# Kernel optimization log

Measured on AMD Instinct MI355X. Metric: run time of the kernel, lower is better.

## Reference

```python
import jax, jax.numpy as jnp
import numpy as np

N, E, G = 200000, 600000, 1024
NF_IN, EF_IN, H = 32, 16, 512
BN_EPS = 1e-5


def _bn(x, gamma, beta):
    # eval-mode BatchNorm1d with running_mean=0, running_var=1
    return x * (gamma / jnp.sqrt(1.0 + BN_EPS)) + beta


def setup_inputs() -> dict:
    key = jax.random.key(0)
    ks = jax.random.split(key, 32)
    s = 0.05
    inp = {
        'nf': jax.random.normal(ks[0], (N, NF_IN), jnp.float32),
        'ef': jax.random.normal(ks[1], (E, EF_IN), jnp.float32),
        'gf': jax.random.normal(ks[2], (G, H), jnp.float32),
        'device_params': jax.random.uniform(ks[3], (N,), jnp.float32),
        'node_y': jax.random.randint(ks[4], (N,), 0, 9),
        'batch_idx': jnp.sort(jax.random.randint(ks[5], (N,), 0, G)),
        'edge_index': jax.random.randint(ks[6], (2, E), 0, N),
        'nf_w1': jax.random.normal(ks[7], (NF_IN + 9, H), jnp.float32) * s,
        'nf_b1': jax.random.normal(ks[8], (H,), jnp.float32) * s,
        'nf_g1': jax.random.uniform(ks[9], (H,), jnp.float32, 0.5, 1.5),
        'nf_be1': jax.random.normal(ks[10], (H,), jnp.float32) * s,
        'nf_w2': jax.random.normal(ks[11], (H, H), jnp.float32) * s,
        'nf_b2': jax.random.normal(ks[12], (H,), jnp.float32) * s,
        'ef_w1': jax.random.normal(ks[13], (EF_IN, H), jnp.float32) * s,
        'ef_b1': jax.random.normal(ks[14], (H,), jnp.float32) * s,
        'ef_g1': jax.random.uniform(ks[15], (H,), jnp.float32, 0.5, 1.5),
        'ef_be1': jax.random.normal(ks[16], (H,), jnp.float32) * s,
        'ef_w2': jax.random.normal(ks[17], (H, H), jnp.float32) * s,
        'ef_b2': jax.random.normal(ks[18], (H,), jnp.float32) * s,
        'ow1': jax.random.normal(ks[19], (H, H), jnp.float32) * s,
        'ob1': jax.random.normal(ks[20], (H,), jnp.float32) * s,
        'og1': jax.random.uniform(ks[21], (H,), jnp.float32, 0.5, 1.5),
        'obe1': jax.random.normal(ks[22], (H,), jnp.float32) * s,
        'ow2': jax.random.normal(ks[23], (H, H), jnp.float32) * s,
        'ob2': jax.random.normal(ks[24], (H,), jnp.float32) * s,
        'og2': jax.random.uniform(ks[25], (H,), jnp.float32, 0.5, 1.5),
        'obe2': jax.random.normal(ks[26], (H,), jnp.float32) * s,
        'ow3': jax.random.normal(ks[27], (H, 2), jnp.float32) * s,
        'ob3': jax.random.normal(ks[28], (2,), jnp.float32) * s,
    }
    return inp


def reference(nf, ef, gf, device_params, node_y, batch_idx, edge_index,
              nf_w1, nf_b1, nf_g1, nf_be1, nf_w2, nf_b2,
              ef_w1, ef_b1, ef_g1, ef_be1, ef_w2, ef_b2,
              ow1, ob1, og1, obe1, ow2, ob2, og2, obe2, ow3, ob3):
    num_graphs = gf.shape[0]
    gelu = lambda x: jax.nn.gelu(x, approximate=False)  # torch nn.GELU default

    # DeviceParam_MLP: augment node features with scaled one-hot of node class
    nf_aug = jnp.concatenate(
        [nf, jax.nn.one_hot(node_y, 9, dtype=nf.dtype) * device_params[:, None]],
        axis=-1)  # [N, nf_in+9]
    h_n = gelu(_bn(nf_aug @ nf_w1 + nf_b1, nf_g1, nf_be1)) @ nf_w2 + nf_b2  # [N,H]
    h_e = gelu(_bn(ef @ ef_w1 + ef_b1, ef_g1, ef_be1)) @ ef_w2 + ef_b2      # [E,H]

    # two scatter_add pools into graph features
    gh = gf
    gh = gh + jax.ops.segment_sum(h_n, batch_idx, num_segments=num_graphs)
    edge_graph = batch_idx[edge_index[0]]  # graph id of each edge's source node
    gh = gh + jax.ops.segment_sum(h_e, edge_graph, num_segments=num_graphs)

    # output MLP (layer_num=3): two hidden blocks + final Linear -> 2
    x = gelu(_bn(gh @ ow1 + ob1, og1, obe1))
    x = gelu(_bn(x @ ow2 + ob2, og2, obe2))
    return x @ ow3 + ob3  # [G, 2]
```

## Files before the change

kernel.cpp:

```cpp
#include <hip/hip_runtime.h>
#include <hip/hip_bf16.h>

#define NN 200000
#define NE 600000
#define NG 1024
#define HH 512
#define ECAP 1024

typedef short short8 __attribute__((ext_vector_type(8)));
typedef float f32x4 __attribute__((ext_vector_type(4)));
typedef float f32x2 __attribute__((ext_vector_type(2)));
typedef float f32x16 __attribute__((ext_vector_type(16)));

__device__ __forceinline__ unsigned short f2bf(float f){
  unsigned u = __float_as_uint(f);
  u += 0x7fffu + ((u >> 16) & 1u);
  return (unsigned short)(u >> 16);
}
__device__ __forceinline__ float bf2f(unsigned short h){
  return __uint_as_float(((unsigned)h) << 16);
}

__device__ __forceinline__ short8 cvt8pk(float4 a, float4 b){
  union { short8 s; __hip_bfloat162 h[4]; } u;
  u.h[0] = __float22bfloat162_rn(make_float2(a.x, a.y));
  u.h[1] = __float22bfloat162_rn(make_float2(a.z, a.w));
  u.h[2] = __float22bfloat162_rn(make_float2(b.x, b.y));
  u.h[3] = __float22bfloat162_rn(make_float2(b.z, b.w));
  return u.s;
}

__device__ __forceinline__ void split8(const float* v, short8* hi, short8* lo){
  union { short8 s; __hip_bfloat162 h[4]; unsigned u[4]; } H, L;
#pragma unroll
  for (int p=0;p<4;++p){
    float a = v[2*p], b = v[2*p+1];
    H.h[p] = __float22bfloat162_rn(make_float2(a, b));
    unsigned hu = H.u[p];
    L.h[p] = __float22bfloat162_rn(make_float2(a - __uint_as_float(hu << 16),
                                               b - __uint_as_float(hu & 0xffff0000u)));
  }
  *hi = H.s; *lo = L.s;
}

__device__ __forceinline__ float gelu_f(float x){
  float p = __builtin_fmaf(x*x, -0.10294325f, -2.3022085f);
  float e = __builtin_amdgcn_exp2f(x * p);
  return x * __builtin_amdgcn_rcpf(1.0f + e);
}

__device__ __forceinline__ void g2(f32x2 xp, f32x2& aX, f32x2& aP,
    float C0, float C1, float C2, float C3, float C4, float C5, float C6, float C7){
  f32x2 s = __builtin_elementwise_fma(xp, xp, (f32x2)(-1.0f));
  f32x2 p = __builtin_elementwise_fma(s, (f32x2)C7, (f32x2)C6);
  p = __builtin_elementwise_fma(p, s, (f32x2)C5);
  p = __builtin_elementwise_fma(p, s, (f32x2)C4);
  p = __builtin_elementwise_fma(p, s, (f32x2)C3);
  p = __builtin_elementwise_fma(p, s, (f32x2)C2);
  p = __builtin_elementwise_fma(p, s, (f32x2)C1);
  p = __builtin_elementwise_fma(p, s, (f32x2)C0);
  aX += xp; aP += p;
}

#define ISQ 0.35355339059327376f
#define SQ2 1.41421356237309505f

__global__ __launch_bounds__(256) void kpre(
    const float* __restrict__ nfw1, const float* __restrict__ nfb1,
    const float* __restrict__ nfg1, const float* __restrict__ nfbe1,
    const float* __restrict__ efw1, const float* __restrict__ efb1,
    const float* __restrict__ efg1, const float* __restrict__ efbe1,
    unsigned short* __restrict__ w1n48T, unsigned short* __restrict__ w1eT16,
    float* __restrict__ b1n_s, float* __restrict__ b1e_s,
    const int* __restrict__ bidx, int* __restrict__ nstart,
    int* __restrict__ cnt, float* __restrict__ pcoef,
    const float* __restrict__ nf, const float* __restrict__ dp,
    const int* __restrict__ ny, const float* __restrict__ ef,
    unsigned short* __restrict__ nf48, unsigned short* __restrict__ efb){
  const float rs = 0.99999500003750f;
  int b = blockIdx.x, t = threadIdx.x;
  if (b < 2){
    int c = b*256 + t;
    float sc = efg1[c]*rs*ISQ;
#pragma unroll
    for (int k=0;k<16;++k) w1eT16[c*16+k] = f2bf(efw1[k*HH+c]*sc);
    b1e_s[c] = (efb1[c]*efg1[c]*rs + efbe1[c])*ISQ;
  } else if (b < 4){
    int c = (b-2)*256 + t;
    float sc = nfg1[c]*rs*ISQ;
#pragma unroll
    for (int k=0;k<48;++k)
      w1n48T[c*48+k] = (k < 41) ? f2bf(nfw1[k*HH+c]*sc) : (unsigned short)0;
    b1n_s[c] = (nfb1[c]*nfg1[c]*rs + nfbe1[c])*ISQ;
  } else if (b < 786){
    int i = (b-4)*256 + t;
    if (i < NN){
      int g0 = bidx[i];
      int g1 = (i+1 < NN) ? bidx[i+1] : NG;
      for (int g = g0+1; g <= g1; ++g) nstart[g] = i+1;
      if (i == 0) for (int g = 0; g <= g0; ++g) nstart[g] = 0;
    }
  } else if (b == 786){
    cnt[t] = 0; cnt[t+256] = 0; cnt[t+512] = 0; cnt[t+768] = 0;
    if (t == 0){
      double th[8], fj[8];
      for (int j=0;j<8;++j){
        th[j] = 3.14159265358979323846*((double)j + 0.5)/8.0;
        double cs = cos(th[j]);
        double u = 8.0*(cs + 1.0);
        double v = sqrt(u);
        fj[j] = 0.5*v*erf(v*0.70710678118654752);
      }
      double c[8];
      for (int k=0;k<8;++k){
        double sm = 0.0;
        for (int j=0;j<8;++j) sm += fj[j]*cos((double)k*th[j]);
        c[k] = 0.25*sm;
      }
      c[0] *= 0.5;
      const double T[8][8] = {
        { 1, 0,  0,  0,   0,    0,  0,  0},
        { 0, 1,  0,  0,   0,    0,  0,  0},
        {-1, 0,  2,  0,   0,    0,  0,  0},
        { 0,-3,  0,  4,   0,    0,  0,  0},
        { 1, 0, -8,  0,   8,    0,  0,  0},
        { 0, 5,  0,-20,   0,   16,  0,  0},
        {-1, 0, 18,  0, -48,    0, 32,  0},
        { 0,-7,  0, 56,   0, -112,  0, 64}};
      double m[8] = {0,0,0,0,0,0,0,0};
      for (int k=0;k<8;++k)
        for (int i=0;i<8;++i) m[i] += c[k]*T[k][i];
      double p0 = m[0]-m[1]+m[2]-m[3]+m[4]-m[5]+m[6]-m[7];
      m[0] -= p0;
      for (int i=0;i<8;++i) pcoef[i] = (float)m[i];
    }
  } else if (b < 1569){
    int r = (b-787)*256 + t;
    if (r < NN){
      const float4* ap = (const float4*)(nf + (size_t)r*32);
      unsigned short v[48];
      union { short8 s; unsigned short u[8]; } cv;
#pragma unroll
      for (int p2=0; p2<4; ++p2){
        cv.s = cvt8pk(ap[2*p2], ap[2*p2+1]);
#pragma unroll
        for (int j=0;j<8;++j) v[p2*8+j] = cv.u[j];
      }
      unsigned short db = f2bf(dp[r]);
      int cls = ny[r];
#pragma unroll
      for (int j=0;j<9;++j) v[32+j] = (cls==j) ? db : (unsigned short)0;
#pragma unroll
      for (int j=41;j<48;++j) v[j] = 0;
      unsigned short* op = nf48 + (size_t)r*48;
#pragma unroll
      for (int p2=0; p2<6; ++p2) *(short8*)(op + p2*8) = *(short8*)&v[p2*8];
    }
  } else {
    int r = (b-1569)*256 + t;
    if (r < NE){
      const float4* ap = (const float4*)(ef + (size_t)r*16);
      unsigned short* op = efb + (size_t)r*16;
      *(short8*)op       = cvt8pk(ap[0], ap[1]);
      *(short8*)(op + 8) = cvt8pk(ap[2], ap[3]);
    }
  }
}

__global__ __launch_bounds__(1024) void kscatter(const int* __restrict__ eidx,
    const int* __restrict__ bidx, int* __restrict__ eg,
    int* __restrict__ cnt, int* __restrict__ perm2d){
  __shared__ int h[NG];
  __shared__ int base[NG];
  const int b = blockIdx.x, t = threadIdx.x;
  h[t] = 0;
  __syncthreads();
  const int per = NE / 64;
  const int lo = b*per, hi = lo + per;
  for (int e = lo + t; e < hi; e += 1024){
    int g = bidx[eidx[e]];
    eg[e] = g;
    atomicAdd(&h[g], 1);
  }
  __syncthreads();
  int c = h[t];
  if (c > 0) base[t] = atomicAdd(&cnt[t], c);
  h[t] = 0;
  __syncthreads();
  for (int e = lo + t; e < hi; e += 1024){
    int g = eg[e];
    int p = base[g] + atomicAdd(&h[g], 1);
    if (p < ECAP) perm2d[(g << 10) + p] = e;
  }
}

__global__ __launch_bounds__(512) void kedge(
    const unsigned short* __restrict__ efb, const int* __restrict__ perm2d,
    const int* __restrict__ cnt, const unsigned short* __restrict__ w1eT16,
    const float* __restrict__ b1e_s, const float* __restrict__ pcoef,
    float* __restrict__ S){
  __shared__ short lds[2][32*40];
  const int t = threadIdx.x;
  const int lane = t & 63, wid = t >> 6;
  const int hi = lane >> 5;
  const int g = blockIdx.x >> 1;
  const int col = ((blockIdx.x & 1) << 8) + (wid << 5) + (lane & 31);
  const float C0 = pcoef[0], C1 = pcoef[1], C2 = pcoef[2], C3 = pcoef[3];
  const float C4 = pcoef[4], C5 = pcoef[5], C6 = pcoef[6], C7 = pcoef[7];
  short8 bfr = *(const short8*)(w1eT16 + col*16 + (hi<<3));
  float bv = b1e_s[col];
  f32x16 bias16;
#pragma unroll
  for (int i=0;i<16;++i) bias16[i] = bv;
  f32x2 aX = {0.f,0.f}, aP = {0.f,0.f};
  const int s1 = cnt[g];
  if (s1 > 0){
    const int base = g << 10;
    const int nch = (s1 + 31) >> 5;
    short8 a1;
    if (t < 64){
      int r0 = min(t & 31, s1-1);
      int r1 = min(32 + (t & 31), s1-1);
      int e0 = perm2d[base + r0];
      int e1 = perm2d[base + r1];
      short8 a0 = *(const short8*)(efb + (size_t)e0*16 + ((t>>5)<<3));
      *(short8*)&lds[0][(t&31)*40 + ((t>>5)<<3)] = a0;
      a1 = *(const short8*)(efb + (size_t)e1*16 + ((t>>5)<<3));
    }
    __syncthreads();
    for (int ch=0; ch<nch; ++ch){
      short8 af = *(const short8*)&lds[ch&1][(lane&31)*40 + (hi<<3)];
      if (t < 64){
        if (ch+1 < nch) *(short8*)&lds[(ch+1)&1][(t&31)*40 + ((t>>5)<<3)] = a1;
        int r2 = min((ch+2)*32 + (t & 31), s1-1);
        int e2 = perm2d[base + r2];
        a1 = *(const short8*)(efb + (size_t)e2*16 + ((t>>5)<<3));
      }
      __syncthreads();
      f32x16 acc = __builtin_amdgcn_mfma_f32_32x32x16_bf16(af, bfr, bias16, 0, 0, 0);
      const int vr = s1 - ch*32;
      if (vr >= 32){
#pragma unroll
        for (int i=0;i<8;++i){
          f32x2 xp = {acc[2*i], acc[2*i+1]};
          g2(xp, aX, aP, C0,C1,C2,C3,C4,C5,C6,C7);
        }
      } else {
#pragma unroll
        for (int i=0;i<8;++i){
          int r0 = ((2*i)&3) + (((2*i)>>2)<<3) + (hi<<2);
          f32x2 xp = { (r0 < vr) ? acc[2*i] : 0.f,
                       (r0+1 < vr) ? acc[2*i+1] : 0.f };
          g2(xp, aX, aP, C0,C1,C2,C3,C4,C5,C6,C7);
        }
      }
    }
  }
  float ssum = __builtin_fmaf(SQ2, aX[0]+aX[1], aP[0]+aP[1]);
  ssum += __shfl_xor(ssum, 32);
  if (lane < 32) S[(size_t)g*1024 + 512 + col] = ssum;
}

__global__ __launch_bounds__(256) void knode(
    const unsigned short* __restrict__ nf48, const int* __restrict__ nstart,
    const unsigned short* __restrict__ w1n48T, const float* __restrict__ b1n_s,
    const float* __restrict__ pcoef, float* __restrict__ S){
  const int t = threadIdx.x;
  const int lane = t & 63, wid = t >> 6;
  const int hi = lane >> 5;
  const int g = blockIdx.x >> 2;
  const int col = ((blockIdx.x & 3) << 7) + (wid << 5) + (lane & 31);
  const float C0 = pcoef[0], C1 = pcoef[1], C2 = pcoef[2], C3 = pcoef[3];
  const float C4 = pcoef[4], C5 = pcoef[5], C6 = pcoef[6], C7 = pcoef[7];
  const unsigned short* bp = w1n48T + col*48 + (hi<<3);
  short8 bf0 = *(const short8*)(bp);
  short8 bf1 = *(const short8*)(bp + 16);
  short8 bf2 = *(const short8*)(bp + 32);
  float bv = b1n_s[col];
  f32x16 bias16;
#pragma unroll
  for (int i=0;i<16;++i) bias16[i] = bv;
  f32x2 aX = {0.f,0.f}, aP = {0.f,0.f};
  const int s0 = nstart[g], s1 = nstart[g+1];
  const int nch = (s1 - s0 + 31) >> 5;
  for (int ch=0; ch<nch; ++ch){
    int rb = s0 + ch*32;
    int ar = min(rb + (lane & 31), s1-1);
    const unsigned short* apn = nf48 + (size_t)ar*48 + (hi<<3);
    short8 a0 = *(const short8*)(apn);
    short8 a1 = *(const short8*)(apn + 16);
    short8 a2 = *(const short8*)(apn + 32);
    f32x16 acc = __builtin_amdgcn_mfma_f32_32x32x16_bf16(a0, bf0, bias16, 0, 0, 0);
    acc = __builtin_amdgcn_mfma_f32_32x32x16_bf16(a1, bf1, acc, 0, 0, 0);
    acc = __builtin_amdgcn_mfma_f32_32x32x16_bf16(a2, bf2, acc, 0, 0, 0);
    const int vr = s1 - rb;
    if (vr >= 32){
#pragma unroll
      for (int i=0;i<8;++i){
        f32x2 xp = {acc[2*i], acc[2*i+1]};
        g2(xp, aX, aP, C0,C1,C2,C3,C4,C5,C6,C7);
      }
    } else {
#pragma unroll
      for (int i=0;i<8;++i){
        int r0 = ((2*i)&3) + (((2*i)>>2)<<3) + (hi<<2);
        f32x2 xp = { (r0 < vr) ? acc[2*i] : 0.f,
                     (r0+1 < vr) ? acc[2*i+1] : 0.f };
        g2(xp, aX, aP, C0,C1,C2,C3,C4,C5,C6,C7);
      }
    }
  }
  float ssum = __builtin_fmaf(SQ2, aX[0]+aX[1], aP[0]+aP[1]);
  ssum += __shfl_xor(ssum, 32);
  if (lane < 32) S[(size_t)g*1024 + col] = ssum;
}

__global__ __launch_bounds__(256) void kgemm3(const float* __restrict__ A, int lda, int nkc,
    const float* __restrict__ B0, const float* __restrict__ B1,
    float* __restrict__ out,
    const float* __restrict__ gf, const int* __restrict__ nstart, const int* __restrict__ cnt,
    const float* __restrict__ b2n, const float* __restrict__ b2e,
    const float* __restrict__ bias, const float* __restrict__ gam, const float* __restrict__ bet){
  const int t = threadIdx.x, lane = t & 63, w = t >> 6;
  const int q = lane >> 4, m = lane & 15;
  const int c0 = blockIdx.x*16, r0 = blockIdx.y*64 + w*16;
  f32x4 acc = {0.f,0.f,0.f,0.f};
  const float* ap = A + (size_t)(r0 + m)*lda + (q<<3);
  for (int kc = 0; kc < nkc; ++kc){
    const int ko = kc*32;
    float4 x = *(const float4*)(ap + ko);
    float4 y = *(const float4*)(ap + ko + 4);
    float v[8] = {x.x,x.y,x.z,x.w,y.x,y.y,y.z,y.w};
    short8 ah, al;
    split8(v, &ah, &al);
    const float* Bp = (kc < 16) ? B0 : B1;
    const float* bp = Bp + (size_t)((kc & 15)*32 + (q<<3))*HH + c0 + m;
    float bvv[8];
#pragma unroll
    for (int j=0;j<8;++j) bvv[j] = bp[(size_t)j*HH];
    short8 bh, bl;
    split8(bvv, &bh, &bl);
    acc = __builtin_amdgcn_mfma_f32_16x16x32_bf16(ah, bh, acc, 0, 0, 0);
    acc = __builtin_amdgcn_mfma_f32_16x16x32_bf16(ah, bl, acc, 0, 0, 0);
    acc = __builtin_amdgcn_mfma_f32_16x16x32_bf16(al, bh, acc, 0, 0, 0);
  }
  const float rs = 0.99999500003750f;
  const int c = c0 + m;
  if (gf){
    const float bnv = b2n[c], bev = b2e[c];
#pragma unroll
    for (int i=0;i<4;++i){
      int r = r0 + q*4 + i;
      float cn = (float)(nstart[r+1] - nstart[r]);
      float ce = (float)cnt[r];
      out[(size_t)r*HH + c] = acc[i] + gf[(size_t)r*HH + c] + cn*bnv + ce*bev;
    }
  } else {
    const float sc = gam[c]*rs, bi = bias[c], be = bet[c];
#pragma unroll
    for (int i=0;i<4;++i){
      int r = r0 + q*4 + i;
      out[(size_t)r*HH + c] = gelu_f((acc[i] + bi)*sc + be);
    }
  }
}

__global__ __launch_bounds__(256) void kfinal(const float* __restrict__ x2, const float* __restrict__ w3,
    const float* __restrict__ b3, float* __restrict__ out){
  const int lane = threadIdx.x & 63, wv = threadIdx.x >> 6;
  const int r = blockIdx.x*4 + wv;
  float a0 = 0.f, a1 = 0.f;
#pragma unroll
  for (int tt=0; tt<8; ++tt){
    int k = lane + tt*64;
    float x = x2[(size_t)r*HH + k];
    a0 = __builtin_fmaf(x, w3[2*k], a0);
    a1 = __builtin_fmaf(x, w3[2*k+1], a1);
  }
#pragma unroll
  for (int d=1; d<64; d<<=1){ a0 += __shfl_xor(a0, d); a1 += __shfl_xor(a1, d); }
  if (lane == 0){ out[r*2] = a0 + b3[0]; out[r*2+1] = a1 + b3[1]; }
}

extern "C" void kernel_launch(void* const* d_in, const int* in_sizes, int n_in,
                              void* d_out, int out_size, void* d_ws, size_t ws_size,
                              hipStream_t stream) {
  const float* nf    = (const float*)d_in[0];
  const float* ef    = (const float*)d_in[1];
  const float* gf    = (const float*)d_in[2];
  const float* dp    = (const float*)d_in[3];
  const int*   ny    = (const int*)d_in[4];
  const int*   bidx  = (const int*)d_in[5];
  const int*   eidx  = (const int*)d_in[6];
  const float* nfw1  = (const float*)d_in[7];
  const float* nfb1  = (const float*)d_in[8];
  const float* nfg1  = (const float*)d_in[9];
  const float* nfbe1 = (const float*)d_in[10];
  const float* w2n   = (const float*)d_in[11];
  const float* b2n   = (const float*)d_in[12];
  const float* efw1  = (const float*)d_in[13];
  const float* efb1  = (const float*)d_in[14];
  const float* efg1  = (const float*)d_in[15];
  const float* efbe1 = (const float*)d_in[16];
  const float* w2e   = (const float*)d_in[17];
  const float* b2e   = (const float*)d_in[18];
  const float* ow1   = (const float*)d_in[19];
  const float* ob1   = (const float*)d_in[20];
  const float* og1   = (const float*)d_in[21];
  const float* obe1  = (const float*)d_in[22];
  const float* ow2   = (const float*)d_in[23];
  const float* ob2   = (const float*)d_in[24];
  const float* og2   = (const float*)d_in[25];
  const float* obe2  = (const float*)d_in[26];
  const float* ow3   = (const float*)d_in[27];
  const float* ob3   = (const float*)d_in[28];

  unsigned char* p = (unsigned char*)d_ws;
  float* S      = (float*)p;                 p += (size_t)NG*1024*4;
  int*   perm2d = (int*)p;                   p += (size_t)NG*ECAP*4;
  unsigned short* nf48 = (unsigned short*)p; p += (size_t)NN*48*2;
  unsigned short* efb  = (unsigned short*)p; p += (size_t)NE*16*2;
  unsigned short* w1n48T = (unsigned short*)p; p += 512*48*2;
  unsigned short* w1eT16 = (unsigned short*)p; p += 512*16*2;
  float* b1n_s  = (float*)p;                 p += 512*4;
  float* b1e_s  = (float*)p;                 p += 512*4;
  int* nstart   = (int*)p;                   p += 1032*4;
  int* cnt      = (int*)p;                   p += NG*4;
  float* pcoef  = (float*)p;                 p += 64;
  int* eg = (int*)S;
  float* gh  = (float*)nf48;
  float* xg2 = gh  + (size_t)NG*HH;
  float* x2f = xg2 + (size_t)NG*HH;

  kpre<<<3913, 256, 0, stream>>>(nfw1, nfb1, nfg1, nfbe1, efw1, efb1, efg1, efbe1,
                                 w1n48T, w1eT16, b1n_s, b1e_s, bidx, nstart, cnt,
                                 pcoef, nf, dp, ny, ef, nf48, efb);
  kscatter<<<64, 1024, 0, stream>>>(eidx, bidx, eg, cnt, perm2d);
  kedge<<<2048, 512, 0, stream>>>(efb, perm2d, cnt, w1eT16, b1e_s, pcoef, S);
  knode<<<4096, 256, 0, stream>>>(nf48, nstart, w1n48T, b1n_s, pcoef, S);
  kgemm3<<<dim3(32,16), 256, 0, stream>>>(S, 1024, 32, w2n, w2e, gh,
                                          gf, nstart, cnt, b2n, b2e,
                                          nullptr, nullptr, nullptr);
  kgemm3<<<dim3(32,16), 256, 0, stream>>>(gh, 512, 16, ow1, ow1, xg2,
                                          nullptr, nullptr, nullptr, nullptr, nullptr,
                                          ob1, og1, obe1);
  kgemm3<<<dim3(32,16), 256, 0, stream>>>(xg2, 512, 16, ow2, ow2, x2f,
                                          nullptr, nullptr, nullptr, nullptr, nullptr,
                                          ob2, og2, obe2);
  kfinal<<<NG/4, 256, 0, stream>>>(x2f, ow3, ob3, (float*)d_out);
}
```

Baseline: 341.1 us.

## Process two column tiles per wave and use packed FMA asm for GELU sums

The edge and node pooling kernels now launch one block per graph. Each wave covers two 32-column tiles, so every gathered A fragment feeds two MFMAs and the edge/row loads are amortised. The LDS double-buffered prefetch in the edge kernel is replaced by direct per-wave gathers. Bias is added after the MFMA through packed adds, and the GELU polynomial uses inline v_pk_fma_f32 asm. The trade-offs are fewer blocks in flight, more registers per wave, and the loss of explicit prefetch latency hiding in the edge path.

```diff
diff --git a/kernel.cpp b/kernel.cpp
--- a/kernel.cpp
+++ b/kernel.cpp
@@ -49,18 +49,34 @@
   return x * __builtin_amdgcn_rcpf(1.0f + e);
 }
 
-__device__ __forceinline__ void g2(f32x2 xp, f32x2& aX, f32x2& aP,
-    float C0, float C1, float C2, float C3, float C4, float C5, float C6, float C7){
-  f32x2 s = __builtin_elementwise_fma(xp, xp, (f32x2)(-1.0f));
-  f32x2 p = __builtin_elementwise_fma(s, (f32x2)C7, (f32x2)C6);
-  p = __builtin_elementwise_fma(p, s, (f32x2)C5);
-  p = __builtin_elementwise_fma(p, s, (f32x2)C4);
-  p = __builtin_elementwise_fma(p, s, (f32x2)C3);
-  p = __builtin_elementwise_fma(p, s, (f32x2)C2);
-  p = __builtin_elementwise_fma(p, s, (f32x2)C1);
-  p = __builtin_elementwise_fma(p, s, (f32x2)C0);
-  aX += xp; aP += p;
-}
+#define PKFMA(d,a,b,c) asm("v_pk_fma_f32 %0, %1, %2, %3" : "=v"(d) : "v"(a), "v"(b), "v"(c))
+#define PKADD(d,a,b)   asm("v_pk_add_f32 %0, %1, %2"     : "=v"(d) : "v"(a), "v"(b))
+
+#define G2B(xp_, b2_) { \
+  f32x2 y_; PKADD(y_, xp_, b2_); \
+  f32x2 s_; PKFMA(s_, y_, y_, n1); \
+  f32x2 p_; PKFMA(p_, s_, K7, K6); \
+  PKFMA(p_, p_, s_, K5); PKFMA(p_, p_, s_, K4); \
+  PKFMA(p_, p_, s_, K3); PKFMA(p_, p_, s_, K2); \
+  PKFMA(p_, p_, s_, K1); PKFMA(p_, p_, s_, K0); \
+  PKADD(aX, aX, y_); PKADD(aP, aP, p_); }
+
+#define G2BM(xp_, b2_, ok0_, ok1_) { \
+  f32x2 y_; PKADD(y_, xp_, b2_); \
+  y_[0] = (ok0_) ? y_[0] : 0.f; y_[1] = (ok1_) ? y_[1] : 0.f; \
+  f32x2 s_; PKFMA(s_, y_, y_, n1); \
+  f32x2 p_; PKFMA(p_, s_, K7, K6); \
+  PKFMA(p_, p_, s_, K5); PKFMA(p_, p_, s_, K4); \
+  PKFMA(p_, p_, s_, K3); PKFMA(p_, p_, s_, K2); \
+  PKFMA(p_, p_, s_, K1); PKFMA(p_, p_, s_, K0); \
+  PKADD(aX, aX, y_); PKADD(aP, aP, p_); }
+
+#define COEFS \
+  const float C0 = pcoef[0], C1 = pcoef[1], C2 = pcoef[2], C3 = pcoef[3]; \
+  const float C4 = pcoef[4], C5 = pcoef[5], C6 = pcoef[6], C7 = pcoef[7]; \
+  const f32x2 K0 = {C0,C0}, K1 = {C1,C1}, K2 = {C2,C2}, K3 = {C3,C3}; \
+  const f32x2 K4 = {C4,C4}, K5 = {C5,C5}, K6 = {C6,C6}, K7 = {C7,C7}; \
+  const f32x2 n1 = {-1.f,-1.f};
 
 #define ISQ 0.35355339059327376f
 #define SQ2 1.41421356237309505f
@@ -199,120 +215,158 @@
     const int* __restrict__ cnt, const unsigned short* __restrict__ w1eT16,
     const float* __restrict__ b1e_s, const float* __restrict__ pcoef,
     float* __restrict__ S){
-  __shared__ short lds[2][32*40];
   const int t = threadIdx.x;
   const int lane = t & 63, wid = t >> 6;
   const int hi = lane >> 5;
-  const int g = blockIdx.x >> 1;
-  const int col = ((blockIdx.x & 1) << 8) + (wid << 5) + (lane & 31);
-  const float C0 = pcoef[0], C1 = pcoef[1], C2 = pcoef[2], C3 = pcoef[3];
-  const float C4 = pcoef[4], C5 = pcoef[5], C6 = pcoef[6], C7 = pcoef[7];
-  short8 bfr = *(const short8*)(w1eT16 + col*16 + (hi<<3));
-  float bv = b1e_s[col];
-  f32x16 bias16;
-#pragma unroll
-  for (int i=0;i<16;++i) bias16[i] = bv;
+  const int g = blockIdx.x;
+  const int col = (wid << 6) + (lane & 31);
+  COEFS;
+  short8 bfr0 = *(const short8*)(w1eT16 + col*16 + (hi<<3));
+  short8 bfr1 = *(const short8*)(w1eT16 + (col+32)*16 + (hi<<3));
+  float bv0 = b1e_s[col], bv1 = b1e_s[col+32];
+  const f32x2 b20 = {bv0,bv0}, b21 = {bv1,bv1};
+  f32x16 z16;
+#pragma unroll
+  for (int i=0;i<16;++i) z16[i] = 0.f;
   f32x2 aX = {0.f,0.f}, aP = {0.f,0.f};
-  const int s1 = cnt[g];
-  if (s1 > 0){
-    const int base = g << 10;
-    const int nch = (s1 + 31) >> 5;
-    short8 a1;
-    if (t < 64){
-      int r0 = min(t & 31, s1-1);
-      int r1 = min(32 + (t & 31), s1-1);
-      int e0 = perm2d[base + r0];
-      int e1 = perm2d[base + r1];
-      short8 a0 = *(const short8*)(efb + (size_t)e0*16 + ((t>>5)<<3));
-      *(short8*)&lds[0][(t&31)*40 + ((t>>5)<<3)] = a0;
-      a1 = *(const short8*)(efb + (size_t)e1*16 + ((t>>5)<<3));
-    }
-    __syncthreads();
-    for (int ch=0; ch<nch; ++ch){
-      short8 af = *(const short8*)&lds[ch&1][(lane&31)*40 + (hi<<3)];
-      if (t < 64){
-        if (ch+1 < nch) *(short8*)&lds[(ch+1)&1][(t&31)*40 + ((t>>5)<<3)] = a1;
-        int r2 = min((ch+2)*32 + (t & 31), s1-1);
-        int e2 = perm2d[base + r2];
-        a1 = *(const short8*)(efb + (size_t)e2*16 + ((t>>5)<<3));
-      }
-      __syncthreads();
-      f32x16 acc = __builtin_amdgcn_mfma_f32_32x32x16_bf16(af, bfr, bias16, 0, 0, 0);
-      const int vr = s1 - ch*32;
-      if (vr >= 32){
-#pragma unroll
-        for (int i=0;i<8;++i){
-          f32x2 xp = {acc[2*i], acc[2*i+1]};
-          g2(xp, aX, aP, C0,C1,C2,C3,C4,C5,C6,C7);
-        }
-      } else {
-#pragma unroll
-        for (int i=0;i<8;++i){
-          int r0 = ((2*i)&3) + (((2*i)>>2)<<3) + (hi<<2);
-          f32x2 xp = { (r0 < vr) ? acc[2*i] : 0.f,
-                       (r0+1 < vr) ? acc[2*i+1] : 0.f };
-          g2(xp, aX, aP, C0,C1,C2,C3,C4,C5,C6,C7);
-        }
-      }
-    }
-  }
-  float ssum = __builtin_fmaf(SQ2, aX[0]+aX[1], aP[0]+aP[1]);
-  ssum += __shfl_xor(ssum, 32);
-  if (lane < 32) S[(size_t)g*1024 + 512 + col] = ssum;
-}
-
-__global__ __launch_bounds__(256) void knode(
+  f32x2 aX1 = {0.f,0.f}, aP1 = {0.f,0.f};
+  const int s1 = min(cnt[g], ECAP);
+  const int base = g << 10;
+  const int nch = (s1 + 31) >> 5;
+  for (int ch=0; ch<nch; ++ch){
+    const int rb = ch*32;
+    int e = perm2d[base + min(rb + (lane & 31), s1-1)];
+    short8 af = *(const short8*)(efb + (size_t)e*16 + (hi<<3));
+    f32x16 acc0 = __builtin_amdgcn_mfma_f32_32x32x16_bf16(af, bfr0, z16, 0, 0, 0);
+    f32x16 acc1 = __builtin_amdgcn_mfma_f32_32x32x16_bf16(af, bfr1, z16, 0, 0, 0);
+    const int vr = s1 - rb;
+    if (vr >= 32){
+#pragma unroll
+      for (int i=0;i<8;++i){
+        f32x2 xp = {acc0[2*i], acc0[2*i+1]};
+        G2B(xp, b20);
+      }
+#pragma unroll
+      for (int i=0;i<8;++i){
+        f32x2 xp = {acc1[2*i], acc1[2*i+1]};
+        { f32x2 y_; PKADD(y_, xp, b21);
+          f32x2 s_; PKFMA(s_, y_, y_, n1);
+          f32x2 p_; PKFMA(p_, s_, K7, K6);
+          PKFMA(p_, p_, s_, K5); PKFMA(p_, p_, s_, K4);
+          PKFMA(p_, p_, s_, K3); PKFMA(p_, p_, s_, K2);
+          PKFMA(p_, p_, s_, K1); PKFMA(p_, p_, s_, K0);
+          PKADD(aX1, aX1, y_); PKADD(aP1, aP1, p_); }
+      }
+    } else {
+#pragma unroll
+      for (int i=0;i<8;++i){
+        int r0 = ((2*i)&3) + (((2*i)>>2)<<3) + (hi<<2);
+        bool ok0 = r0 < vr, ok1 = (r0+1) < vr;
+        f32x2 xp = {acc0[2*i], acc0[2*i+1]};
+        G2BM(xp, b20, ok0, ok1);
+        f32x2 xq = {acc1[2*i], acc1[2*i+1]};
+        { f32x2 y_; PKADD(y_, xq, b21);
+          y_[0] = ok0 ? y_[0] : 0.f; y_[1] = ok1 ? y_[1] : 0.f;
+          f32x2 s_; PKFMA(s_, y_, y_, n1);
+          f32x2 p_; PKFMA(p_, s_, K7, K6);
+          PKFMA(p_, p_, s_, K5); PKFMA(p_, p_, s_, K4);
+          PKFMA(p_, p_, s_, K3); PKFMA(p_, p_, s_, K2);
+          PKFMA(p_, p_, s_, K1); PKFMA(p_, p_, s_, K0);
+          PKADD(aX1, aX1, y_); PKADD(aP1, aP1, p_); }
+      }
+    }
+  }
+  float s0 = __builtin_fmaf(SQ2, aX[0]+aX[1], aP[0]+aP[1]);
+  float s1v = __builtin_fmaf(SQ2, aX1[0]+aX1[1], aP1[0]+aP1[1]);
+  s0 += __shfl_xor(s0, 32);
+  s1v += __shfl_xor(s1v, 32);
+  if (lane < 32){
+    S[(size_t)g*1024 + 512 + col] = s0;
+    S[(size_t)g*1024 + 512 + col + 32] = s1v;
+  }
+}
+
+__global__ __launch_bounds__(512) void knode(
     const unsigned short* __restrict__ nf48, const int* __restrict__ nstart,
     const unsigned short* __restrict__ w1n48T, const float* __restrict__ b1n_s,
     const float* __restrict__ pcoef, float* __restrict__ S){
   const int t = threadIdx.x;
   const int lane = t & 63, wid = t >> 6;
   const int hi = lane >> 5;
-  const int g = blockIdx.x >> 2;
-  const int col = ((blockIdx.x & 3) << 7) + (wid << 5) + (lane & 31);
-  const float C0 = pcoef[0], C1 = pcoef[1], C2 = pcoef[2], C3 = pcoef[3];
-  const float C4 = pcoef[4], C5 = pcoef[5], C6 = pcoef[6], C7 = pcoef[7];
-  const unsigned short* bp = w1n48T + col*48 + (hi<<3);
-  short8 bf0 = *(const short8*)(bp);
-  short8 bf1 = *(const short8*)(bp + 16);
-  short8 bf2 = *(const short8*)(bp + 32);
-  float bv = b1n_s[col];
-  f32x16 bias16;
-#pragma unroll
-  for (int i=0;i<16;++i) bias16[i] = bv;
+  const int g = blockIdx.x;
+  const int col = (wid << 6) + (lane & 31);
+  COEFS;
+  const unsigned short* bp0 = w1n48T + col*48 + (hi<<3);
+  const unsigned short* bp1 = w1n48T + (col+32)*48 + (hi<<3);
+  short8 b00 = *(const short8*)(bp0), b01 = *(const short8*)(bp0+16), b02 = *(const short8*)(bp0+32);
+  short8 b10 = *(const short8*)(bp1), b11 = *(const short8*)(bp1+16), b12 = *(const short8*)(bp1+32);
+  float bv0 = b1n_s[col], bv1 = b1n_s[col+32];
+  const f32x2 b20 = {bv0,bv0}, b21 = {bv1,bv1};
+  f32x16 z16;
+#pragma unroll
+  for (int i=0;i<16;++i) z16[i] = 0.f;
   f32x2 aX = {0.f,0.f}, aP = {0.f,0.f};
-  const int s0 = nstart[g], s1 = nstart[g+1];
-  const int nch = (s1 - s0 + 31) >> 5;
+  f32x2 aX1 = {0.f,0.f}, aP1 = {0.f,0.f};
+  const int s0r = nstart[g], s1 = nstart[g+1];
+  const int nch = (s1 - s0r + 31) >> 5;
   for (int ch=0; ch<nch; ++ch){
-    int rb = s0 + ch*32;
+    const int rb = s0r + ch*32;
     int ar = min(rb + (lane & 31), s1-1);
     const unsigned short* apn = nf48 + (size_t)ar*48 + (hi<<3);
     short8 a0 = *(const short8*)(apn);
     short8 a1 = *(const short8*)(apn + 16);
     short8 a2 = *(const short8*)(apn + 32);
-    f32x16 acc = __builtin_amdgcn_mfma_f32_32x32x16_bf16(a0, bf0, bias16, 0, 0, 0);
-    acc = __builtin_amdgcn_mfma_f32_32x32x16_bf16(a1, bf1, acc, 0, 0, 0);
-    acc = __builtin_amdgcn_mfma_f32_32x32x16_bf16(a2, bf2, acc, 0, 0, 0);
+    f32x16 acc0 = __builtin_amdgcn_mfma_f32_32x32x16_bf16(a0, b00, z16, 0, 0, 0);
+    acc0 = __builtin_amdgcn_mfma_f32_32x32x16_bf16(a1, b01, acc0, 0, 0, 0);
+    acc0 = __builtin_amdgcn_mfma_f32_32x32x16_bf16(a2, b02, acc0, 0, 0, 0);
+    f32x16 acc1 = __builtin_amdgcn_mfma_f32_32x32x16_bf16(a0, b10, z16, 0, 0, 0);
+    acc1 = __builtin_amdgcn_mfma_f32_32x32x16_bf16(a1, b11, acc1, 0, 0, 0);
+    acc1 = __builtin_amdgcn_mfma_f32_32x32x16_bf16(a2, b12, acc1, 0, 0, 0);
     const int vr = s1 - rb;
     if (vr >= 32){
 #pragma unroll
       for (int i=0;i<8;++i){
-        f32x2 xp = {acc[2*i], acc[2*i+1]};
-        g2(xp, aX, aP, C0,C1,C2,C3,C4,C5,C6,C7);
+        f32x2 xp = {acc0[2*i], acc0[2*i+1]};
+        G2B(xp, b20);
+      }
+#pragma unroll
+      for (int i=0;i<8;++i){
+        f32x2 xp = {acc1[2*i], acc1[2*i+1]};
+        { f32x2 y_; PKADD(y_, xp, b21);
+          f32x2 s_; PKFMA(s_, y_, y_, n1);
+          f32x2 p_; PKFMA(p_, s_, K7, K6);
+          PKFMA(p_, p_, s_, K5); PKFMA(p_, p_, s_, K4);
+          PKFMA(p_, p_, s_, K3); PKFMA(p_, p_, s_, K2);
+          PKFMA(p_, p_, s_, K1); PKFMA(p_, p_, s_, K0);
+          PKADD(aX1, aX1, y_); PKADD(aP1, aP1, p_); }
       }
     } else {
 #pragma unroll
       for (int i=0;i<8;++i){
         int r0 = ((2*i)&3) + (((2*i)>>2)<<3) + (hi<<2);
-        f32x2 xp = { (r0 < vr) ? acc[2*i] : 0.f,
-                     (r0+1 < vr) ? acc[2*i+1] : 0.f };
-        g2(xp, aX, aP, C0,C1,C2,C3,C4,C5,C6,C7);
-      }
-    }
-  }
-  float ssum = __builtin_fmaf(SQ2, aX[0]+aX[1], aP[0]+aP[1]);
-  ssum += __shfl_xor(ssum, 32);
-  if (lane < 32) S[(size_t)g*1024 + col] = ssum;
+        bool ok0 = r0 < vr, ok1 = (r0+1) < vr;
+        f32x2 xp = {acc0[2*i], acc0[2*i+1]};
+        G2BM(xp, b20, ok0, ok1);
+        f32x2 xq = {acc1[2*i], acc1[2*i+1]};
+        { f32x2 y_; PKADD(y_, xq, b21);
+          y_[0] = ok0 ? y_[0] : 0.f; y_[1] = ok1 ? y_[1] : 0.f;
+          f32x2 s_; PKFMA(s_, y_, y_, n1);
+          f32x2 p_; PKFMA(p_, s_, K7, K6);
+          PKFMA(p_, p_, s_, K5); PKFMA(p_, p_, s_, K4);
+          PKFMA(p_, p_, s_, K3); PKFMA(p_, p_, s_, K2);
+          PKFMA(p_, p_, s_, K1); PKFMA(p_, p_, s_, K0);
+          PKADD(aX1, aX1, y_); PKADD(aP1, aP1, p_); }
+      }
+    }
+  }
+  float r0s = __builtin_fmaf(SQ2, aX[0]+aX[1], aP[0]+aP[1]);
+  float r1s = __builtin_fmaf(SQ2, aX1[0]+aX1[1], aP1[0]+aP1[1]);
+  r0s += __shfl_xor(r0s, 32);
+  r1s += __shfl_xor(r1s, 32);
+  if (lane < 32){
+    S[(size_t)g*1024 + col] = r0s;
+    S[(size_t)g*1024 + col + 32] = r1s;
+  }
 }
 
 __global__ __launch_bounds__(256) void kgemm3(const float* __restrict__ A, int lda, int nkc,
@@ -436,8 +490,8 @@
                                  w1n48T, w1eT16, b1n_s, b1e_s, bidx, nstart, cnt,
                                  pcoef, nf, dp, ny, ef, nf48, efb);
   kscatter<<<64, 1024, 0, stream>>>(eidx, bidx, eg, cnt, perm2d);
-  kedge<<<2048, 512, 0, stream>>>(efb, perm2d, cnt, w1eT16, b1e_s, pcoef, S);
-  knode<<<4096, 256, 0, stream>>>(nf48, nstart, w1n48T, b1n_s, pcoef, S);
+  kedge<<<NG, 512, 0, stream>>>(efb, perm2d, cnt, w1eT16, b1e_s, pcoef, S);
+  knode<<<NG, 512, 0, stream>>>(nf48, nstart, w1n48T, b1n_s, pcoef, S);
   kgemm3<<<dim3(32,16), 256, 0, stream>>>(S, 1024, 32, w2n, w2e, gh,
                                           gf, nstart, cnt, b2n, b2e,
                                           nullptr, nullptr, nullptr);
```

After: 345.0 us. No clear change (+1.1%).
